# Performance work log

Hardware: AMD Instinct MI355X
Metric: run time of the kernel (lower is better)

Reference implementation:

```python
import jax, jax.numpy as jnp
import numpy as np

NUM_HEADS = 16
HEAD_DIM = 64  # dim_qkv // num_heads


def setup_inputs() -> dict:
    key = jax.random.key(0)
    ks = jax.random.split(key, 6)
    B, N, D = 2, 2048, 1024
    s = 1.0 / np.sqrt(D)
    x = jax.random.normal(ks[0], (B, N, D), dtype=jnp.float32)
    Wq = jax.random.normal(ks[1], (D, D), dtype=jnp.float32) * s
    Wk = jax.random.normal(ks[2], (D, D), dtype=jnp.float32) * s
    Wv = jax.random.normal(ks[3], (D, D), dtype=jnp.float32) * s
    Wo = jax.random.normal(ks[4], (D, D), dtype=jnp.float32) * s
    z = jnp.zeros((D,), dtype=jnp.float32)
    return {"x": x, "Wq": Wq, "bq": z, "Wk": Wk, "bk": z,
            "Wv": Wv, "bv": z, "Wo": Wo, "bo": z}


def _split_heads(t):
    # [B, N, H*dh] -> [B, H, N, dh]
    B, N, _ = t.shape
    return t.reshape(B, N, NUM_HEADS, HEAD_DIM).transpose(0, 2, 1, 3)


def reference(x, Wq, bq, Wk, bk, Wv, bv, Wo, bo):
    q = _split_heads(x @ Wq + bq)
    k = _split_heads(x @ Wk + bk)
    v = _split_heads(x @ Wv + bv)
    scores = jnp.einsum('bhnd,bhmd->bhnm', q, k) / jnp.sqrt(
        jnp.asarray(HEAD_DIM, dtype=x.dtype))
    attn = jax.nn.softmax(scores, axis=-1)
    heads = jnp.einsum('bhnm,bhmd->bhnd', attn, v)  # [B, H, N, dh]
    B, H, N, dh = heads.shape
    merged = heads.transpose(0, 2, 1, 3).reshape(B, N, H * dh)
    # dropout is identity in deterministic/eval mode
    return merged @ Wo + bo
```

## Files before the change

### kernel.cpp

```cpp
#include <hip/hip_runtime.h>
#include <hip/hip_bf16.h>

typedef __bf16 bf16;
typedef __attribute__((ext_vector_type(8))) __bf16 bf16x8;
typedef __attribute__((ext_vector_type(4))) __bf16 bf16x4;
typedef __attribute__((ext_vector_type(4))) float f32x4;
typedef __attribute__((ext_vector_type(16))) float f32x16;
typedef unsigned int uint;

#define MFMA16(a, b, c) __builtin_amdgcn_mfma_f32_16x16x32_bf16(a, b, c, 0, 0, 0)
#define MFMA32(a, b, c) __builtin_amdgcn_mfma_f32_32x32x16_bf16(a, b, c, 0, 0, 0)

#define GLOAD_LDS(gp, lp) \
  __builtin_amdgcn_global_load_lds( \
      (const __attribute__((address_space(1))) void*)(gp), \
      (__attribute__((address_space(3))) void*)(lp), 16, 0, 0)

#define QSCALE 0.18033688011112042f

__device__ __forceinline__ uint pack2(float a, float b) {
  unsigned short x = __builtin_bit_cast(unsigned short, (bf16)a);
  unsigned short y = __builtin_bit_cast(unsigned short, (bf16)b);
  return (uint)x | ((uint)y << 16);
}

__global__ __launch_bounds__(256) void prep_kernel(
    const float* __restrict__ x, bf16* __restrict__ y,
    const float* __restrict__ W0, const float* __restrict__ W1,
    const float* __restrict__ W2, const float* __restrict__ W3,
    bf16* __restrict__ T0, bf16* __restrict__ T1,
    bf16* __restrict__ T2, bf16* __restrict__ T3) {
  const int bid = blockIdx.x;
  if (bid < 2048) {
    int i = (bid * 256 + threadIdx.x) * 8;
    float4 a = *(const float4*)(x + i);
    float4 b = *(const float4*)(x + i + 4);
    bf16x8 v;
    v[0] = (bf16)a.x; v[1] = (bf16)a.y; v[2] = (bf16)a.z; v[3] = (bf16)a.w;
    v[4] = (bf16)b.x; v[5] = (bf16)b.y; v[6] = (bf16)b.z; v[7] = (bf16)b.w;
    *(bf16x8*)(y + i) = v;
    return;
  }
  const int wq = bid - 2048;
  const int z = wq >> 10, rem = wq & 1023;
  const float* W; bf16* T;
  switch (z) {
    case 0: W = W0; T = T0; break;
    case 1: W = W1; T = T1; break;
    case 2: W = W2; T = T2; break;
    default: W = W3; T = T3; break;
  }
  const float scl = (z == 0) ? QSCALE : 1.0f;
  __shared__ float tile[32][33];
  int tx = threadIdx.x & 31;
  int ty = threadIdx.x >> 5;
  int bx = (rem & 31) * 32, by = (rem >> 5) * 32;
#pragma unroll
  for (int i = 0; i < 32; i += 8)
    tile[ty + i][tx] = W[(size_t)(by + ty + i) * 1024 + bx + tx];
  __syncthreads();
#pragma unroll
  for (int i = 0; i < 32; i += 8)
    T[(size_t)(bx + ty + i) * 1024 + by + tx] = (bf16)(tile[tx][ty + i] * scl);
}

__global__ __launch_bounds__(256, 2) void gemm_qkv_kernel(
    const bf16* __restrict__ A, const bf16* __restrict__ Bt,
    const float* __restrict__ b0, const float* __restrict__ b1,
    const float* __restrict__ b2, bf16* __restrict__ o0,
    bf16* __restrict__ o1, bf16* __restrict__ o2) {
  __shared__ bf16 As[128 * 64];
  __shared__ bf16 Bs[128 * 64];
  const int f = blockIdx.y * 24 + blockIdx.x;
  const int wg = (f % 8) * 96 + f / 8;
  const int bn = wg % 24, bm = wg / 24;
  const int t = threadIdx.x;
  const int lane = t & 63, wid = t >> 6;
  const int wy = wid >> 1, wx = wid & 1;
  const int lr = lane & 15, lg = lane >> 4;
  const bf16* Arow = A + (size_t)bm * 128 * 1024;
  const bf16* Brow = Bt + (size_t)bn * 128 * 1024;
  f32x4 acc[4][4] = {};

  for (int k0 = 0; k0 < 1024; k0 += 64) {
    __syncthreads();
#pragma unroll
    for (int i = 0; i < 4; i++) {
      int off = i * 256 + t;
      int row = off >> 3, ch = off & 7;
      int gch = ch ^ (row & 7);
      GLOAD_LDS(Arow + (size_t)row * 1024 + k0 + gch * 8, As + off * 8);
    }
#pragma unroll
    for (int i = 0; i < 4; i++) {
      int off = i * 256 + t;
      int row = off >> 3, ch = off & 7;
      int gch = ch ^ (row & 7);
      GLOAD_LDS(Brow + (size_t)row * 1024 + k0 + gch * 8, Bs + off * 8);
    }
    __syncthreads();
#pragma unroll
    for (int kh = 0; kh < 2; kh++) {
      bf16x8 af[4], bfr[4];
#pragma unroll
      for (int i = 0; i < 4; i++) {
        int row = wy * 64 + i * 16 + lr;
        int c = kh * 4 + lg;
        af[i] = *(const bf16x8*)(As + row * 64 + ((c ^ (row & 7)) << 3));
      }
#pragma unroll
      for (int j = 0; j < 4; j++) {
        int row = wx * 64 + j * 16 + lr;
        int c = kh * 4 + lg;
        bfr[j] = *(const bf16x8*)(Bs + row * 64 + ((c ^ (row & 7)) << 3));
      }
#pragma unroll
      for (int i = 0; i < 4; i++)
#pragma unroll
        for (int j = 0; j < 4; j++)
          acc[i][j] = MFMA16(af[i], bfr[j], acc[i][j]);
    }
  }

  const int seg = bn >> 3;
  const float* bias = (seg == 0) ? b0 : (seg == 1 ? b1 : b2);
  const float bscale = (seg == 0) ? QSCALE : 1.0f;

#pragma unroll
  for (int i = 0; i < 4; i++) {
    const int rowb = bm * 128 + wy * 64 + i * 16 + lg * 4;
#pragma unroll
    for (int j = 0; j < 4; j++) {
      const int np = bn * 128 + wx * 64 + j * 16 + lr;
      const int col = np & 1023;
      const float bv = bias[col] * bscale;
      const int h = col >> 6, d = col & 63;
      const int bb = rowb >> 11, nn = rowb & 2047;
      if (seg == 2) {
        bf16x4 pk;
#pragma unroll
        for (int r = 0; r < 4; r++) pk[r] = (bf16)(acc[i][j][r] + bv);
        *(bf16x4*)(o2 + (((size_t)bb * 16 + h) * 64 + d) * 2048 + nn) = pk;
      } else {
        bf16* dst = (seg == 0) ? o0 : o1;
#pragma unroll
        for (int r = 0; r < 4; r++)
          dst[(((size_t)bb * 16 + h) * 2048 + nn + r) * 64 + d] =
              (bf16)(acc[i][j][r] + bv);
      }
    }
  }
}

__global__ __launch_bounds__(256, 2) void gemmo_kernel(
    const bf16* __restrict__ A, const bf16* __restrict__ Bt,
    const float* __restrict__ bias, float* __restrict__ out) {
  __shared__ bf16 As[128 * 64];
  __shared__ bf16 Bs[64 * 64];
  const int f = blockIdx.y * 16 + blockIdx.x;
  const int wg = (f & 7) * 64 + (f >> 3);
  const int bn = wg & 15, bm = wg >> 4;
  const int t = threadIdx.x;
  const int lane = t & 63, wid = t >> 6;
  const int wy = wid >> 1, wx = wid & 1;
  const int lr = lane & 15, lg = lane >> 4;
  const bf16* Arow = A + (size_t)bm * 128 * 1024;
  const bf16* Brow = Bt + (size_t)bn * 64 * 1024;
  f32x4 acc[4][2] = {};

  for (int k0 = 0; k0 < 1024; k0 += 64) {
    __syncthreads();
#pragma unroll
    for (int i = 0; i < 4; i++) {
      int off = i * 256 + t;
      int row = off >> 3, ch = off & 7;
      int gch = ch ^ (row & 7);
      GLOAD_LDS(Arow + (size_t)row * 1024 + k0 + gch * 8, As + off * 8);
    }
#pragma unroll
    for (int i = 0; i < 2; i++) {
      int off = i * 256 + t;
      int row = off >> 3, ch = off & 7;
      int gch = ch ^ (row & 7);
      GLOAD_LDS(Brow + (size_t)row * 1024 + k0 + gch * 8, Bs + off * 8);
    }
    __syncthreads();
#pragma unroll
    for (int kh = 0; kh < 2; kh++) {
      bf16x8 af[4], bfr[2];
#pragma unroll
      for (int i = 0; i < 4; i++) {
        int row = wy * 64 + i * 16 + lr;
        int c = kh * 4 + lg;
        af[i] = *(const bf16x8*)(As + row * 64 + ((c ^ (row & 7)) << 3));
      }
#pragma unroll
      for (int j = 0; j < 2; j++) {
        int row = wx * 32 + j * 16 + lr;
        int c = kh * 4 + lg;
        bfr[j] = *(const bf16x8*)(Bs + row * 64 + ((c ^ (row & 7)) << 3));
      }
#pragma unroll
      for (int i = 0; i < 4; i++)
#pragma unroll
        for (int j = 0; j < 2; j++)
          acc[i][j] = MFMA16(af[i], bfr[j], acc[i][j]);
    }
  }

#pragma unroll
  for (int i = 0; i < 4; i++) {
    const int rowb = bm * 128 + wy * 64 + i * 16 + lg * 4;
#pragma unroll
    for (int j = 0; j < 2; j++) {
      const int col = bn * 64 + wx * 32 + j * 16 + lr;
      const float bv = bias[col];
#pragma unroll
      for (int r = 0; r < 4; r++)
        out[(size_t)(rowb + r) * 1024 + col] = acc[i][j][r] + bv;
    }
  }
}

__global__ __launch_bounds__(256, 2) void attn_kernel(
    const bf16* __restrict__ Q, const bf16* __restrict__ K,
    const bf16* __restrict__ Vt, bf16* __restrict__ Mg) {
  __shared__ bf16 Kl[2][8192];
  __shared__ bf16 Vl[2][8192];
  const int t = threadIdx.x;
  const int lane = t & 63, w = t >> 6;
  const int l31 = lane & 31, hi = lane >> 5;
  const int f = blockIdx.y * 16 + blockIdx.x;
  const int xcd = f & 7, slot = f >> 3;
  const int bh = xcd * 4 + (slot >> 4);
  const int bx = slot & 15;
  const int b = bh >> 4, h = bh & 15;
  const bf16* Qh = Q + (size_t)bh * 2048 * 64;
  const bf16* Kh = K + (size_t)bh * 2048 * 64;
  const bf16* Vh = Vt + (size_t)bh * 64 * 2048;
  const int q_row = bx * 128 + w * 32 + l31;

  bf16x8 qf[4];
#pragma unroll
  for (int dblk = 0; dblk < 4; dblk++)
    qf[dblk] = *(const bf16x8*)(Qh + (size_t)q_row * 64 + dblk * 16 + hi * 8);

  bf16x8 onesA;
  {
    bf16 ov = (l31 == 0) ? (bf16)1.0f : (bf16)0.0f;
#pragma unroll
    for (int e = 0; e < 8; e++) onesA[e] = ov;
  }

  f32x16 o0 = {}, o1 = {}, osum = {};

#define STAGE(kt_, buf_)                                                      \
  {                                                                           \
    _Pragma("unroll") for (int i = 0; i < 4; i++) {                           \
      int off = i * 256 + t;                                                  \
      int row = off >> 3, ch = off & 7;                                       \
      int gch = ch ^ (row & 7);                                               \
      GLOAD_LDS(Kh + (size_t)(kt_) * 8192 + row * 64 + gch * 8,               \
                &Kl[buf_][off * 8]);                                          \
    }                                                                         \
    _Pragma("unroll") for (int i = 0; i < 4; i++) {                           \
      int off = i * 256 + t;                                                  \
      int row = off >> 4, ch = off & 15;                                      \
      int gch = ch ^ (row & 15);                                              \
      GLOAD_LDS(Vh + (size_t)row * 2048 + (kt_) * 128 + gch * 8,              \
                &Vl[buf_][off * 8]);                                          \
    }                                                                         \
  }

  STAGE(0, 0);
  __syncthreads();

  for (int kt = 0; kt < 16; kt++) {
    const int cur = kt & 1;
    if (kt < 15) STAGE(kt + 1, cur ^ 1);

#pragma unroll
    for (int hf = 0; hf < 2; hf++) {
      f32x16 s0 = {}, s1 = {};
      __builtin_amdgcn_s_setprio(1);
#pragma unroll
      for (int dblk = 0; dblk < 4; dblk++) {
        const int c = dblk * 2 + hi;
        const int r0 = hf * 64 + l31, r1 = hf * 64 + 32 + l31;
        bf16x8 kf0 = *(const bf16x8*)&Kl[cur][r0 * 64 + ((c ^ (r0 & 7)) << 3)];
        bf16x8 kf1 = *(const bf16x8*)&Kl[cur][r1 * 64 + ((c ^ (r1 & 7)) << 3)];
        s0 = MFMA32(kf0, qf[dblk], s0);
        s1 = MFMA32(kf1, qf[dblk], s1);
      }
      __builtin_amdgcn_s_setprio(0);

#pragma unroll
      for (int r = 0; r < 16; r++) {
        s0[r] = __builtin_amdgcn_exp2f(s0[r]);
        s1[r] = __builtin_amdgcn_exp2f(s1[r]);
      }

      uint prc[8], prd[8];
#pragma unroll
      for (int si = 0; si < 4; si++) {
        prc[si] = pack2(s0[4 * si + 0], s0[4 * si + 1]);
        prd[si] = pack2(s0[4 * si + 2], s0[4 * si + 3]);
        prc[4 + si] = pack2(s1[4 * si + 0], s1[4 * si + 1]);
        prd[4 + si] = pack2(s1[4 * si + 2], s1[4 * si + 3]);
      }

      __builtin_amdgcn_s_setprio(1);
#pragma unroll
      for (int kbl = 0; kbl < 4; kbl++) {
        const int sb = (kbl >> 1) * 4 + (kbl & 1) * 2;
        auto rc = __builtin_amdgcn_permlane32_swap(prc[sb], prc[sb + 1], false, false);
        auto rd = __builtin_amdgcn_permlane32_swap(prd[sb], prd[sb + 1], false, false);
        union { uint u[4]; bf16x8 v; } pf;
        pf.u[0] = rc[0];
        pf.u[1] = rd[0];
        pf.u[2] = rc[1];
        pf.u[3] = rd[1];

        const int c = (hf * 4 + kbl) * 2 + hi;
        bf16x8 vt0 = *(const bf16x8*)&Vl[cur][l31 * 128 + ((c ^ (l31 & 15)) << 3)];
        bf16x8 vt1 =
            *(const bf16x8*)&Vl[cur][(32 + l31) * 128 + ((c ^ ((32 + l31) & 15)) << 3)];
        o0 = MFMA32(vt0, pf.v, o0);
        o1 = MFMA32(vt1, pf.v, o1);
        osum = MFMA32(onesA, pf.v, osum);
      }
      __builtin_amdgcn_s_setprio(0);
    }

    __syncthreads();
  }

  uint lu = __builtin_bit_cast(uint, osum[0]);
  auto lb = __builtin_amdgcn_permlane32_swap(lu, lu, false, false);
  const float inv = 1.f / __builtin_bit_cast(float, (uint)lb[0]);

  bf16* orow = Mg + ((size_t)b * 2048 + q_row) * 1024 + h * 64;
#pragma unroll
  for (int si = 0; si < 4; si++) {
    bf16x4 p0, p1;
#pragma unroll
    for (int r = 0; r < 4; r++) {
      p0[r] = (bf16)(o0[4 * si + r] * inv);
      p1[r] = (bf16)(o1[4 * si + r] * inv);
    }
    *(bf16x4*)(orow + si * 8 + hi * 4) = p0;
    *(bf16x4*)(orow + 32 + si * 8 + hi * 4) = p1;
  }
}

extern "C" void kernel_launch(void* const* d_in, const int* in_sizes, int n_in,
                              void* d_out, int out_size, void* d_ws, size_t ws_size,
                              hipStream_t stream) {
  const float* x  = (const float*)d_in[0];
  const float* Wq = (const float*)d_in[1];
  const float* bq = (const float*)d_in[2];
  const float* Wk = (const float*)d_in[3];
  const float* bk = (const float*)d_in[4];
  const float* Wv = (const float*)d_in[5];
  const float* bv = (const float*)d_in[6];
  const float* Wo = (const float*)d_in[7];
  const float* bo = (const float*)d_in[8];
  float* out = (float*)d_out;
  char* ws = (char*)d_ws;
  const size_t MiB = 1u << 20;

  bf16* Xb   = (bf16*)(ws);
  bf16* Mg   = Xb;
  bf16* Wqkv = (bf16*)(ws + 8 * MiB);
  bf16* WoT  = (bf16*)(ws + 14 * MiB);
  bf16* Qb   = (bf16*)(ws + 16 * MiB);
  bf16* Kb   = (bf16*)(ws + 24 * MiB);
  bf16* Vtb  = (bf16*)(ws + 32 * MiB);

  prep_kernel<<<6144, 256, 0, stream>>>(
      x, Xb, Wq, Wk, Wv, Wo, Wqkv, Wqkv + (1u << 20), Wqkv + (2u << 20), WoT);
  gemm_qkv_kernel<<<dim3(24, 32), 256, 0, stream>>>(
      Xb, Wqkv, bq, bk, bv, Qb, Kb, Vtb);
  attn_kernel<<<dim3(16, 32), 256, 0, stream>>>(Qb, Kb, Vtb, Mg);
  gemmo_kernel<<<dim3(16, 32), 256, 0, stream>>>(Mg, WoT, bo, out);
  (void)in_sizes; (void)n_in; (void)out_size; (void)ws_size;
}
```

Baseline: 111.6 us.

## Split attention KV range across two wave groups and merge partial sums

After: 110.2 us. No clear change (-1.3%).

```diff
diff --git a/kernel.cpp b/kernel.cpp
--- a/kernel.cpp
+++ b/kernel.cpp
@@ -222,13 +222,14 @@
   }
 }
 
-__global__ __launch_bounds__(256, 2) void attn_kernel(
+__global__ __launch_bounds__(512, 4) void attn_kernel(
     const bf16* __restrict__ Q, const bf16* __restrict__ K,
     const bf16* __restrict__ Vt, bf16* __restrict__ Mg) {
-  __shared__ bf16 Kl[2][8192];
-  __shared__ bf16 Vl[2][8192];
+  __shared__ bf16 Kl[2][2][4096];
+  __shared__ bf16 Vl[2][2][4096];
   const int t = threadIdx.x;
   const int lane = t & 63, w = t >> 6;
+  const int half = w >> 2, wq = w & 3;
   const int l31 = lane & 31, hi = lane >> 5;
   const int f = blockIdx.y * 16 + blockIdx.x;
   const int xcd = f & 7, slot = f >> 3;
@@ -236,9 +237,9 @@
   const int bx = slot & 15;
   const int b = bh >> 4, h = bh & 15;
   const bf16* Qh = Q + (size_t)bh * 2048 * 64;
-  const bf16* Kh = K + (size_t)bh * 2048 * 64;
-  const bf16* Vh = Vt + (size_t)bh * 64 * 2048;
-  const int q_row = bx * 128 + w * 32 + l31;
+  const bf16* KhH = K + (size_t)bh * 2048 * 64 + (size_t)half * 1024 * 64;
+  const bf16* VhH = Vt + (size_t)bh * 64 * 2048 + half * 1024;
+  const int q_row = bx * 128 + wq * 32 + l31;
 
   bf16x8 qf[4];
 #pragma unroll
@@ -253,22 +254,18 @@
   }
 
   f32x16 o0 = {}, o1 = {}, osum = {};
+  const int th = t & 255;
 
 #define STAGE(kt_, buf_)                                                      \
   {                                                                           \
-    _Pragma("unroll") for (int i = 0; i < 4; i++) {                           \
-      int off = i * 256 + t;                                                  \
+    _Pragma("unroll") for (int i = 0; i < 2; i++) {                           \
+      int off = i * 256 + th;                                                 \
       int row = off >> 3, ch = off & 7;                                       \
       int gch = ch ^ (row & 7);                                               \
-      GLOAD_LDS(Kh + (size_t)(kt_) * 8192 + row * 64 + gch * 8,               \
-                &Kl[buf_][off * 8]);                                          \
-    }                                                                         \
-    _Pragma("unroll") for (int i = 0; i < 4; i++) {                           \
-      int off = i * 256 + t;                                                  \
-      int row = off >> 4, ch = off & 15;                                      \
-      int gch = ch ^ (row & 15);                                              \
-      GLOAD_LDS(Vh + (size_t)row * 2048 + (kt_) * 128 + gch * 8,              \
-                &Vl[buf_][off * 8]);                                          \
+      GLOAD_LDS(KhH + (size_t)(kt_) * 4096 + row * 64 + gch * 8,              \
+                &Kl[half][buf_][off * 8]);                                    \
+      GLOAD_LDS(VhH + (size_t)row * 2048 + (kt_) * 64 + gch * 8,              \
+                &Vl[half][buf_][off * 8]);                                    \
     }                                                                         \
   }
 
@@ -279,77 +276,89 @@
     const int cur = kt & 1;
     if (kt < 15) STAGE(kt + 1, cur ^ 1);
 
-#pragma unroll
-    for (int hf = 0; hf < 2; hf++) {
-      f32x16 s0 = {}, s1 = {};
-      __builtin_amdgcn_s_setprio(1);
-#pragma unroll
-      for (int dblk = 0; dblk < 4; dblk++) {
-        const int c = dblk * 2 + hi;
-        const int r0 = hf * 64 + l31, r1 = hf * 64 + 32 + l31;
-        bf16x8 kf0 = *(const bf16x8*)&Kl[cur][r0 * 64 + ((c ^ (r0 & 7)) << 3)];
-        bf16x8 kf1 = *(const bf16x8*)&Kl[cur][r1 * 64 + ((c ^ (r1 & 7)) << 3)];
-        s0 = MFMA32(kf0, qf[dblk], s0);
-        s1 = MFMA32(kf1, qf[dblk], s1);
-      }
-      __builtin_amdgcn_s_setprio(0);
-
-#pragma unroll
-      for (int r = 0; r < 16; r++) {
-        s0[r] = __builtin_amdgcn_exp2f(s0[r]);
-        s1[r] = __builtin_amdgcn_exp2f(s1[r]);
-      }
-
-      uint prc[8], prd[8];
-#pragma unroll
-      for (int si = 0; si < 4; si++) {
-        prc[si] = pack2(s0[4 * si + 0], s0[4 * si + 1]);
-        prd[si] = pack2(s0[4 * si + 2], s0[4 * si + 3]);
-        prc[4 + si] = pack2(s1[4 * si + 0], s1[4 * si + 1]);
-        prd[4 + si] = pack2(s1[4 * si + 2], s1[4 * si + 3]);
-      }
-
-      __builtin_amdgcn_s_setprio(1);
-#pragma unroll
-      for (int kbl = 0; kbl < 4; kbl++) {
-        const int sb = (kbl >> 1) * 4 + (kbl & 1) * 2;
-        auto rc = __builtin_amdgcn_permlane32_swap(prc[sb], prc[sb + 1], false, false);
-        auto rd = __builtin_amdgcn_permlane32_swap(prd[sb], prd[sb + 1], false, false);
-        union { uint u[4]; bf16x8 v; } pf;
-        pf.u[0] = rc[0];
-        pf.u[1] = rd[0];
-        pf.u[2] = rc[1];
-        pf.u[3] = rd[1];
-
-        const int c = (hf * 4 + kbl) * 2 + hi;
-        bf16x8 vt0 = *(const bf16x8*)&Vl[cur][l31 * 128 + ((c ^ (l31 & 15)) << 3)];
-        bf16x8 vt1 =
-            *(const bf16x8*)&Vl[cur][(32 + l31) * 128 + ((c ^ ((32 + l31) & 15)) << 3)];
-        o0 = MFMA32(vt0, pf.v, o0);
-        o1 = MFMA32(vt1, pf.v, o1);
-        osum = MFMA32(onesA, pf.v, osum);
-      }
-      __builtin_amdgcn_s_setprio(0);
-    }
+    f32x16 s0 = {}, s1 = {};
+    __builtin_amdgcn_s_setprio(1);
+#pragma unroll
+    for (int dblk = 0; dblk < 4; dblk++) {
+      const int c = dblk * 2 + hi;
+      const int r0 = l31, r1 = 32 + l31;
+      bf16x8 kf0 = *(const bf16x8*)&Kl[half][cur][r0 * 64 + ((c ^ (r0 & 7)) << 3)];
+      bf16x8 kf1 = *(const bf16x8*)&Kl[half][cur][r1 * 64 + ((c ^ (r1 & 7)) << 3)];
+      s0 = MFMA32(kf0, qf[dblk], s0);
+      s1 = MFMA32(kf1, qf[dblk], s1);
+    }
+    __builtin_amdgcn_s_setprio(0);
+
+#pragma unroll
+    for (int r = 0; r < 16; r++) {
+      s0[r] = __builtin_amdgcn_exp2f(s0[r]);
+      s1[r] = __builtin_amdgcn_exp2f(s1[r]);
+    }
+
+    uint prc[8], prd[8];
+#pragma unroll
+    for (int si = 0; si < 4; si++) {
+      prc[si] = pack2(s0[4 * si + 0], s0[4 * si + 1]);
+      prd[si] = pack2(s0[4 * si + 2], s0[4 * si + 3]);
+      prc[4 + si] = pack2(s1[4 * si + 0], s1[4 * si + 1]);
+      prd[4 + si] = pack2(s1[4 * si + 2], s1[4 * si + 3]);
+    }
+
+    __builtin_amdgcn_s_setprio(1);
+#pragma unroll
+    for (int kbl = 0; kbl < 4; kbl++) {
+      const int sb = (kbl >> 1) * 4 + (kbl & 1) * 2;
+      auto rc = __builtin_amdgcn_permlane32_swap(prc[sb], prc[sb + 1], false, false);
+      auto rd = __builtin_amdgcn_permlane32_swap(prd[sb], prd[sb + 1], false, false);
+      union { uint u[4]; bf16x8 v; } pf;
+      pf.u[0] = rc[0];
+      pf.u[1] = rd[0];
+      pf.u[2] = rc[1];
+      pf.u[3] = rd[1];
+
+      const int c = kbl * 2 + hi;
+      const int r0 = l31, r1 = 32 + l31;
+      bf16x8 vt0 = *(const bf16x8*)&Vl[half][cur][r0 * 64 + ((c ^ (r0 & 7)) << 3)];
+      bf16x8 vt1 = *(const bf16x8*)&Vl[half][cur][r1 * 64 + ((c ^ (r1 & 7)) << 3)];
+      o0 = MFMA32(vt0, pf.v, o0);
+      o1 = MFMA32(vt1, pf.v, o1);
+      osum = MFMA32(onesA, pf.v, osum);
+    }
+    __builtin_amdgcn_s_setprio(0);
 
     __syncthreads();
   }
 
   uint lu = __builtin_bit_cast(uint, osum[0]);
   auto lb = __builtin_amdgcn_permlane32_swap(lu, lu, false, false);
-  const float inv = 1.f / __builtin_bit_cast(float, (uint)lb[0]);
-
-  bf16* orow = Mg + ((size_t)b * 2048 + q_row) * 1024 + h * 64;
-#pragma unroll
-  for (int si = 0; si < 4; si++) {
-    bf16x4 p0, p1;
-#pragma unroll
-    for (int r = 0; r < 4; r++) {
-      p0[r] = (bf16)(o0[4 * si + r] * inv);
-      p1[r] = (bf16)(o1[4 * si + r] * inv);
-    }
-    *(bf16x4*)(orow + si * 8 + hi * 4) = p0;
-    *(bf16x4*)(orow + 32 + si * 8 + hi * 4) = p1;
+  const float den = __builtin_bit_cast(float, (uint)lb[0]);
+
+  float* ma = (float*)&Kl[0][0][0];
+  float* mb = (float*)&Vl[0][0][0];
+  const int mi = (wq * 64 + lane) * 17;
+  if (half == 1) {
+#pragma unroll
+    for (int si = 0; si < 16; si++) {
+      ma[mi + si] = o0[si];
+      mb[mi + si] = o1[si];
+    }
+    ma[mi + 16] = den;
+  }
+  __syncthreads();
+  if (half == 0) {
+    const float inv = 1.f / (den + ma[mi + 16]);
+    bf16* orow = Mg + ((size_t)b * 2048 + q_row) * 1024 + h * 64;
+#pragma unroll
+    for (int si = 0; si < 4; si++) {
+      bf16x4 p0, p1;
+#pragma unroll
+      for (int r = 0; r < 4; r++) {
+        p0[r] = (bf16)((o0[4 * si + r] + ma[mi + 4 * si + r]) * inv);
+        p1[r] = (bf16)((o1[4 * si + r] + mb[mi + 4 * si + r]) * inv);
+      }
+      *(bf16x4*)(orow + si * 8 + hi * 4) = p0;
+      *(bf16x4*)(orow + 32 + si * 8 + hi * 4) = p1;
+    }
   }
 }
 
@@ -381,7 +390,7 @@
       x, Xb, Wq, Wk, Wv, Wo, Wqkv, Wqkv + (1u << 20), Wqkv + (2u << 20), WoT);
   gemm_qkv_kernel<<<dim3(24, 32), 256, 0, stream>>>(
       Xb, Wqkv, bq, bk, bv, Qb, Kb, Vtb);
-  attn_kernel<<<dim3(16, 32), 256, 0, stream>>>(Qb, Kb, Vtb, Mg);
+  attn_kernel<<<dim3(16, 32), 512, 0, stream>>>(Qb, Kb, Vtb, Mg);
   gemmo_kernel<<<dim3(16, 32), 256, 0, stream>>>(Mg, WoT, bo, out);
   (void)in_sizes; (void)n_in; (void)out_size; (void)ws_size;
 }
```

## Triple-buffer 64-key K/V tiles with vmcnt waits in attention kernel

Applied to the files above, without the earlier changes.

Result: no change. 113.2 us (+1.5%).

```diff
diff --git a/kernel.cpp b/kernel.cpp
--- a/kernel.cpp
+++ b/kernel.cpp
@@ -222,14 +222,15 @@
   }
 }
 
-__global__ __launch_bounds__(256, 2) void attn_kernel(
+__global__ __launch_bounds__(256, 3) void attn_kernel(
     const bf16* __restrict__ Q, const bf16* __restrict__ K,
     const bf16* __restrict__ Vt, bf16* __restrict__ Mg) {
-  __shared__ bf16 Kl[2][8192];
-  __shared__ bf16 Vl[2][8192];
+  __shared__ bf16 Kl[3][4096];
+  __shared__ bf16 Vl[3][4096];
   const int t = threadIdx.x;
-  const int lane = t & 63, w = t >> 6;
+  const int lane = t & 63;
   const int l31 = lane & 31, hi = lane >> 5;
+  const int w = t >> 6;
   const int f = blockIdx.y * 16 + blockIdx.x;
   const int xcd = f & 7, slot = f >> 3;
   const int bh = xcd * 4 + (slot >> 4);
@@ -256,88 +257,86 @@
 
 #define STAGE(kt_, buf_)                                                      \
   {                                                                           \
-    _Pragma("unroll") for (int i = 0; i < 4; i++) {                           \
+    _Pragma("unroll") for (int i = 0; i < 2; i++) {                           \
       int off = i * 256 + t;                                                  \
       int row = off >> 3, ch = off & 7;                                       \
       int gch = ch ^ (row & 7);                                               \
-      GLOAD_LDS(Kh + (size_t)(kt_) * 8192 + row * 64 + gch * 8,               \
+      GLOAD_LDS(Kh + (size_t)(kt_) * 4096 + row * 64 + gch * 8,               \
                 &Kl[buf_][off * 8]);                                          \
-    }                                                                         \
-    _Pragma("unroll") for (int i = 0; i < 4; i++) {                           \
-      int off = i * 256 + t;                                                  \
-      int row = off >> 4, ch = off & 15;                                      \
-      int gch = ch ^ (row & 15);                                              \
-      GLOAD_LDS(Vh + (size_t)row * 2048 + (kt_) * 128 + gch * 8,              \
+      GLOAD_LDS(Vh + (size_t)row * 2048 + (kt_) * 64 + gch * 8,               \
                 &Vl[buf_][off * 8]);                                          \
     }                                                                         \
   }
 
   STAGE(0, 0);
-  __syncthreads();
-
-  for (int kt = 0; kt < 16; kt++) {
-    const int cur = kt & 1;
-    if (kt < 15) STAGE(kt + 1, cur ^ 1);
-
-#pragma unroll
-    for (int hf = 0; hf < 2; hf++) {
-      f32x16 s0 = {}, s1 = {};
-      __builtin_amdgcn_s_setprio(1);
-#pragma unroll
-      for (int dblk = 0; dblk < 4; dblk++) {
-        const int c = dblk * 2 + hi;
-        const int r0 = hf * 64 + l31, r1 = hf * 64 + 32 + l31;
-        bf16x8 kf0 = *(const bf16x8*)&Kl[cur][r0 * 64 + ((c ^ (r0 & 7)) << 3)];
-        bf16x8 kf1 = *(const bf16x8*)&Kl[cur][r1 * 64 + ((c ^ (r1 & 7)) << 3)];
-        s0 = MFMA32(kf0, qf[dblk], s0);
-        s1 = MFMA32(kf1, qf[dblk], s1);
-      }
-      __builtin_amdgcn_s_setprio(0);
-
-#pragma unroll
-      for (int r = 0; r < 16; r++) {
-        s0[r] = __builtin_amdgcn_exp2f(s0[r]);
-        s1[r] = __builtin_amdgcn_exp2f(s1[r]);
-      }
-
-      uint prc[8], prd[8];
-#pragma unroll
-      for (int si = 0; si < 4; si++) {
-        prc[si] = pack2(s0[4 * si + 0], s0[4 * si + 1]);
-        prd[si] = pack2(s0[4 * si + 2], s0[4 * si + 3]);
-        prc[4 + si] = pack2(s1[4 * si + 0], s1[4 * si + 1]);
-        prd[4 + si] = pack2(s1[4 * si + 2], s1[4 * si + 3]);
-      }
-
-      __builtin_amdgcn_s_setprio(1);
-#pragma unroll
-      for (int kbl = 0; kbl < 4; kbl++) {
-        const int sb = (kbl >> 1) * 4 + (kbl & 1) * 2;
-        auto rc = __builtin_amdgcn_permlane32_swap(prc[sb], prc[sb + 1], false, false);
-        auto rd = __builtin_amdgcn_permlane32_swap(prd[sb], prd[sb + 1], false, false);
-        union { uint u[4]; bf16x8 v; } pf;
-        pf.u[0] = rc[0];
-        pf.u[1] = rd[0];
-        pf.u[2] = rc[1];
-        pf.u[3] = rd[1];
-
-        const int c = (hf * 4 + kbl) * 2 + hi;
-        bf16x8 vt0 = *(const bf16x8*)&Vl[cur][l31 * 128 + ((c ^ (l31 & 15)) << 3)];
-        bf16x8 vt1 =
-            *(const bf16x8*)&Vl[cur][(32 + l31) * 128 + ((c ^ ((32 + l31) & 15)) << 3)];
-        o0 = MFMA32(vt0, pf.v, o0);
-        o1 = MFMA32(vt1, pf.v, o1);
-        osum = MFMA32(onesA, pf.v, osum);
-      }
-      __builtin_amdgcn_s_setprio(0);
-    }
-
-    __syncthreads();
+  STAGE(1, 1);
+  asm volatile("s_waitcnt vmcnt(4)\n\ts_barrier" ::: "memory");
+
+  for (int kt = 0; kt < 32; kt++) {
+    const int cur = kt % 3;
+    if (kt < 30) STAGE(kt + 2, (kt + 2) % 3);
+
+    f32x16 s0 = {}, s1 = {};
+    __builtin_amdgcn_s_setprio(1);
+#pragma unroll
+    for (int dblk = 0; dblk < 4; dblk++) {
+      const int c = dblk * 2 + hi;
+      const int r0 = l31, r1 = 32 + l31;
+      bf16x8 kf0 = *(const bf16x8*)&Kl[cur][r0 * 64 + ((c ^ (r0 & 7)) << 3)];
+      bf16x8 kf1 = *(const bf16x8*)&Kl[cur][r1 * 64 + ((c ^ (r1 & 7)) << 3)];
+      s0 = MFMA32(kf0, qf[dblk], s0);
+      s1 = MFMA32(kf1, qf[dblk], s1);
+    }
+    __builtin_amdgcn_s_setprio(0);
+
+#pragma unroll
+    for (int r = 0; r < 16; r++) {
+      s0[r] = __builtin_amdgcn_exp2f(s0[r]);
+      s1[r] = __builtin_amdgcn_exp2f(s1[r]);
+    }
+
+    uint prc[8], prd[8];
+#pragma unroll
+    for (int si = 0; si < 4; si++) {
+      prc[si] = pack2(s0[4 * si + 0], s0[4 * si + 1]);
+      prd[si] = pack2(s0[4 * si + 2], s0[4 * si + 3]);
+      prc[4 + si] = pack2(s1[4 * si + 0], s1[4 * si + 1]);
+      prd[4 + si] = pack2(s1[4 * si + 2], s1[4 * si + 3]);
+    }
+
+    __builtin_amdgcn_s_setprio(1);
+#pragma unroll
+    for (int kbl = 0; kbl < 4; kbl++) {
+      const int sb = (kbl >> 1) * 4 + (kbl & 1) * 2;
+      auto rc = __builtin_amdgcn_permlane32_swap(prc[sb], prc[sb + 1], false, false);
+      auto rd = __builtin_amdgcn_permlane32_swap(prd[sb], prd[sb + 1], false, false);
+      union { uint u[4]; bf16x8 v; } pf;
+      pf.u[0] = rc[0];
+      pf.u[1] = rd[0];
+      pf.u[2] = rc[1];
+      pf.u[3] = rd[1];
+
+      const int c = kbl * 2 + hi;
+      const int r0 = l31, r1 = 32 + l31;
+      bf16x8 vt0 = *(const bf16x8*)&Vl[cur][r0 * 64 + ((c ^ (r0 & 7)) << 3)];
+      bf16x8 vt1 = *(const bf16x8*)&Vl[cur][r1 * 64 + ((c ^ (r1 & 7)) << 3)];
+      o0 = MFMA32(vt0, pf.v, o0);
+      o1 = MFMA32(vt1, pf.v, o1);
+      osum = MFMA32(onesA, pf.v, osum);
+    }
+    __builtin_amdgcn_s_setprio(0);
+
+    if (kt < 30) {
+      asm volatile("s_waitcnt vmcnt(4)\n\ts_barrier" ::: "memory");
+    } else if (kt == 30) {
+      asm volatile("s_waitcnt vmcnt(0)\n\ts_barrier" ::: "memory");
+    }
   }
 
   uint lu = __builtin_bit_cast(uint, osum[0]);
   auto lb = __builtin_amdgcn_permlane32_swap(lu, lu, false, false);
-  const float inv = 1.f / __builtin_bit_cast(float, (uint)lb[0]);
+  const float den = hi ? __builtin_bit_cast(float, (uint)lb[0]) : osum[0];
+  const float inv = 1.f / den;
 
   bf16* orow = Mg + ((size_t)b * 2048 + q_row) * 1024 + h * 64;
 #pragma unroll
```
